# Kernel optimization log

Hardware: AMD Instinct MI355X
Metric: run time of the kernel (lower is better)

Reference implementation:

```python
import jax, jax.numpy as jnp
import numpy as np
from jax import lax

B, T = 64, 512
NUM_C = 2000
SK, AN, H, ATT = 256, 96, 256, 80
D = SK + AN  # LSTM input size


def setup_inputs() -> dict:
    key = jax.random.key(0)
    ks = jax.random.split(key, 10)
    s = 0.05
    skill = jax.random.randint(ks[0], (B, T), 0, NUM_C)
    answer = jax.random.randint(ks[1], (B, T), 0, 2)
    skill_emb = jax.random.normal(ks[2], (NUM_C + 1, SK), jnp.float32) * s
    skill_emb = skill_emb.at[-1].set(0.0)  # padding row zeroed as in __init__
    answer_emb = jax.random.normal(ks[3], (3, AN), jnp.float32) * s
    answer_emb = answer_emb.at[-1].set(0.0)
    Wih = jax.random.normal(ks[4], (4 * H, D), jnp.float32) * s
    Whh = jax.random.normal(ks[5], (4 * H, H), jnp.float32) * s
    bih = jnp.zeros((4 * H,), jnp.float32)
    bhh = jnp.zeros((4 * H,), jnp.float32)
    mlp_w = jax.random.normal(ks[6], (ATT, H), jnp.float32) * s
    mlp_b = jnp.zeros((ATT,), jnp.float32)
    sim_w = jax.random.normal(ks[7], (1, ATT), jnp.float32) * s
    fc_w = jax.random.normal(ks[8], (NUM_C, 2 * H), jnp.float32) * s
    fc_b = jnp.zeros((NUM_C,), jnp.float32)
    return dict(skill=skill, answer=answer, skill_emb=skill_emb, answer_emb=answer_emb,
                Wih=Wih, Whh=Whh, bih=bih, bhh=bhh,
                mlp_w=mlp_w, mlp_b=mlp_b, sim_w=sim_w, fc_w=fc_w, fc_b=fc_b)


def _lstm(x, Wih, Whh, bih, bhh):
    # x: [B,T,D] -> h: [B,T,H], PyTorch gate order (i,f,g,o)
    xg = jnp.einsum('btd,gd->btg', x, Wih) + bih + bhh  # precompute input part
    h0 = jnp.zeros((x.shape[0], H), x.dtype)
    c0 = jnp.zeros((x.shape[0], H), x.dtype)

    def step(carry, xt):
        h, c = carry
        g = xt + h @ Whh.T
        i, f, gg, o = jnp.split(g, 4, axis=-1)
        c = jax.nn.sigmoid(f) * c + jax.nn.sigmoid(i) * jnp.tanh(gg)
        h = jax.nn.sigmoid(o) * jnp.tanh(c)
        return (h, c), h

    _, hs = lax.scan(step, (h0, c0), xg.transpose(1, 0, 2))
    return hs.transpose(1, 0, 2)


def reference(skill, answer, skill_emb, answer_emb, Wih, Whh, bih, bhh,
              mlp_w, mlp_b, sim_w, fc_w, fc_b):
    se = skill_emb[skill]    # [B,T,SK]
    ae = answer_emb[answer]  # [B,T,AN]
    sa = jnp.concatenate([se, ae], axis=-1)
    a_s = jnp.concatenate([ae, se], axis=-1)
    sae = jnp.where((answer == 1)[..., None], sa, a_s)  # [B,T,D]

    h = _lstm(sae, Wih, Whh, bih, bhh)  # [B,T,H]

    # rank-1 causal attention: score per timestep, causal softmax == cumulative ratio
    scores = (jnp.tanh(h @ mlp_w.T + mlp_b) @ sim_w.T)[..., 0]  # [B,T]
    m = jnp.max(scores, axis=1, keepdims=True)
    e = jnp.exp(scores - m)                          # [B,T]
    num = jnp.cumsum(e[..., None] * h, axis=1)       # [B,T,H]
    den = jnp.cumsum(e, axis=1)[..., None]           # [B,T,1]
    attn = num / den                                  # == bmm(softmax(masked scores), h)

    cum1 = jnp.cumsum(attn, axis=1) - attn            # exclusive cumsum
    final = jnp.concatenate([cum1, h], axis=-1)       # [B,T,2H]
    res = jax.nn.sigmoid(final @ fc_w.T + fc_b)       # [B,T,num_c]
    return res, sae
```

## Files before the change

### kernel.cpp

```cpp
#include <hip/hip_runtime.h>
#include <hip/hip_fp16.h>

typedef unsigned int  u32;
typedef unsigned short u16;
typedef _Float16 half_t;
typedef _Float16 f16x8 __attribute__((ext_vector_type(8)));
typedef _Float16 h2    __attribute__((ext_vector_type(2)));
typedef float    f32x4 __attribute__((ext_vector_type(4)));

#define B_   64
#define T_   512
#define NUMC 2000
#define H_   256
#define ATT  80
#define D_   352
#define BT_  32768
#define G4   1024

__device__ __forceinline__ float fdot2f(u32 a, u32 b, float c) {
#if __has_builtin(__builtin_amdgcn_fdot2)
  return __builtin_amdgcn_fdot2(__builtin_bit_cast(h2, a), __builtin_bit_cast(h2, b), c, false);
#else
  h2 ha = __builtin_bit_cast(h2, a), hb = __builtin_bit_cast(h2, b);
  return c + (float)ha.x * (float)hb.x + (float)ha.y * (float)hb.y;
#endif
}

__device__ __forceinline__ void load_lds16(const void* g, void* l) {
  __builtin_amdgcn_global_load_lds((const __attribute__((address_space(1))) void*)g,
                                   (__attribute__((address_space(3))) void*)l, 16, 0, 0);
}

__device__ __forceinline__ u32 pack2f(float x, float y) {
  h2 h; h.x = (_Float16)x; h.y = (_Float16)y;
  return __builtin_bit_cast(u32, h);
}

__device__ __forceinline__ float sigmoidf_(float x) { return 1.f / (1.f + __expf(-x)); }

__device__ __forceinline__ float fast_tanhf(float x) {
  float e = __expf(2.f * x);
  return 1.f - 2.f / (e + 1.f);
}

__device__ __forceinline__ int  sel4i(int4 v, int q) { return q==0?v.x:q==1?v.y:q==2?v.z:v.w; }
__device__ __forceinline__ u32  sel4u(uint4 v, int q){ return q==0?v.x:q==1?v.y:q==2?v.z:v.w; }

__global__ void prep_weights(const float* __restrict__ Wih, const float* __restrict__ mlp_w,
                             const float* __restrict__ fc_w,
                             half_t* __restrict__ wih_h, half_t* __restrict__ mlp_p,
                             half_t* __restrict__ fc_p)
{
  int i = blockIdx.x * 256 + threadIdx.x;
  if (i < 360448) { wih_h[i] = (half_t)Wih[i]; return; }
  i -= 360448;
  if (i < 32768) {
    int row = i >> 8;
    mlp_p[i] = (row < ATT) ? (half_t)mlp_w[i] : (half_t)0.f;
    return;
  }
  i -= 32768;
  if (i < 1048576) {
    int row = i >> 9;
    fc_p[i] = (row < NUMC) ? (half_t)fc_w[i] : (half_t)0.f;
  }
}

__global__ __launch_bounds__(128)
void gather_sae(const int* __restrict__ skill, const int* __restrict__ answer,
                const float* __restrict__ semb, const float* __restrict__ aemb,
                float* __restrict__ sae, half_t* __restrict__ sae_h)
{
  const int tok = blockIdx.x;
  const int tid = threadIdx.x;
  const int s = skill[tok], a = answer[tok];
  float* so = sae + (size_t)tok * D_;
  half_t* ho = sae_h + (size_t)tok * D_;
#pragma unroll
  for (int k = 0; k < 3; ++k) {
    int d = tid + k * 128;
    if (d >= D_) break;
    float v;
    if (a == 1) v = (d < 256) ? semb[s * 256 + d]  : aemb[96 + (d - 256)];
    else        v = (d < 96)  ? aemb[a * 96 + d]   : semb[s * 256 + (d - 96)];
    so[d] = v;
    ho[d] = (half_t)v;
  }
}

template<int EPI>
__global__ __launch_bounds__(256)
void gemm_bt(const half_t* __restrict__ A, const half_t* __restrict__ Bm,
             float* __restrict__ Cf, half_t* __restrict__ Ch,
             const float* __restrict__ b0, const float* __restrict__ b1,
             int K, int N, int Nout)
{
  __shared__ half_t At [128 * 32];
  __shared__ half_t Bt2[128 * 32];
  const int tid  = threadIdx.x;
  const int lane = tid & 63;
  const int wv   = tid >> 6;
  const int m0   = blockIdx.x * 128;
  const int n0   = blockIdx.y * 128;
  const int wm   = (wv & 1) * 64, wn = (wv >> 1) * 64;
  const int lrow = wv * 16 + (lane >> 2);
  const int lk   = (lane & 3) * 8;

  f32x4 acc[4][4];
#pragma unroll
  for (int mi = 0; mi < 4; ++mi)
#pragma unroll
    for (int ni = 0; ni < 4; ++ni) acc[mi][ni] = (f32x4){0.f, 0.f, 0.f, 0.f};

  for (int k0 = 0; k0 < K; k0 += 32) {
    load_lds16(A  + (size_t)(m0 + lrow)      * K + k0 + lk, &At [wv * 512]);
    load_lds16(A  + (size_t)(m0 + 64 + lrow) * K + k0 + lk, &At [2048 + wv * 512]);
    load_lds16(Bm + (size_t)(n0 + lrow)      * K + k0 + lk, &Bt2[wv * 512]);
    load_lds16(Bm + (size_t)(n0 + 64 + lrow) * K + k0 + lk, &Bt2[2048 + wv * 512]);
    __syncthreads();
    f16x8 af[4], bf[4];
#pragma unroll
    for (int mi = 0; mi < 4; ++mi)
      af[mi] = *(const f16x8*)&At [(wm + mi * 16 + (lane & 15)) * 32 + (lane >> 4) * 8];
#pragma unroll
    for (int ni = 0; ni < 4; ++ni)
      bf[ni] = *(const f16x8*)&Bt2[(wn + ni * 16 + (lane & 15)) * 32 + (lane >> 4) * 8];
    __syncthreads();
#pragma unroll
    for (int mi = 0; mi < 4; ++mi)
#pragma unroll
      for (int ni = 0; ni < 4; ++ni)
        acc[mi][ni] = __builtin_amdgcn_mfma_f32_16x16x32_f16(af[mi], bf[ni], acc[mi][ni], 0, 0, 0);
  }

  const int rbase = (lane >> 4) * 4;
  const int cidx  = lane & 15;
#pragma unroll
  for (int mi = 0; mi < 4; ++mi) {
#pragma unroll
    for (int ni = 0; ni < 4; ++ni) {
      int gc = n0 + wn + ni * 16 + cidx;
#pragma unroll
      for (int r = 0; r < 4; ++r) {
        int gr = m0 + wm + mi * 16 + rbase + r;
        float v = acc[mi][ni][r];
        if (EPI == 0) {
          Ch[(size_t)gr * N + gc] = (half_t)(v + b0[gc] + b1[gc]);
        } else if (EPI == 1) {
          Cf[(size_t)gr * N + gc] = v;
        } else {
          if (gc < Nout) Cf[(size_t)gr * Nout + gc] = sigmoidf_(v + b0[gc]);
        }
      }
    }
  }
}

#define RPV 96
__global__ __launch_bounds__(512, 2)
void lstm_kernel(const half_t* __restrict__ xg, const float* __restrict__ Whh,
                 u32* __restrict__ hout )
{
  __shared__ uint4 wlds[8 * 1024];
  __shared__ float gbuf[1024];
  __shared__ __align__(16) u16 hq[256];
  const int tid  = threadIdx.x;
  const int lane = tid & 63;
  const int b    = blockIdx.x;
  const int j0   = tid, j1 = tid + 512;

  u32 wA[RPV], wB[RPV];
#pragma unroll
  for (int p = 0; p < RPV; ++p) {
    float2 a = *(const float2*)&Whh[j0 * 256 + 2 * p];
    float2 c = *(const float2*)&Whh[j1 * 256 + 2 * p];
    wA[p] = pack2f(a.x, a.y);
    wB[p] = pack2f(c.x, c.y);
  }
#pragma unroll
  for (int g = 0; g < 8; ++g) {
    const float* pa = &Whh[j0 * 256 + 2 * (RPV + 4 * g)];
    const float* pb = &Whh[j1 * 256 + 2 * (RPV + 4 * g)];
    uint4 wa, wb;
    wa.x = pack2f(pa[0], pa[1]); wa.y = pack2f(pa[2], pa[3]);
    wa.z = pack2f(pa[4], pa[5]); wa.w = pack2f(pa[6], pa[7]);
    wb.x = pack2f(pb[0], pb[1]); wb.y = pack2f(pb[2], pb[3]);
    wb.z = pack2f(pb[4], pb[5]); wb.w = pack2f(pb[6], pb[7]);
    wlds[g * 1024 + j0] = wa;
    wlds[g * 1024 + j1] = wb;
  }
  if (tid < 128) ((u32*)hq)[tid] = 0u;
  float cst = 0.f;
  const half_t* xrow = xg + (size_t)b * T_ * G4;
  float x0 = (float)xrow[j0], x1 = (float)xrow[j1];
  __syncthreads();

  for (int t = 0; t < T_; ++t) {
    int4 hv = ((const int4*)hq)[lane & 31];
    float acc0 = x0, acc1 = x1;
    if (t < T_ - 1) {
      x0 = (float)xrow[(size_t)(t + 1) * G4 + j0];
      x1 = (float)xrow[(size_t)(t + 1) * G4 + j1];
    }
#pragma unroll
    for (int p = 0; p < RPV; ++p) {
      u32 hp = (u32)__builtin_amdgcn_readlane(sel4i(hv, p & 3), p >> 2);
      acc0 = fdot2f(hp, wA[p], acc0);
      acc1 = fdot2f(hp, wB[p], acc1);
    }
#pragma unroll
    for (int g = 0; g < 8; ++g) {
      uint4 wa = wlds[g * 1024 + j0];
      uint4 wb = wlds[g * 1024 + j1];
#pragma unroll
      for (int q = 0; q < 4; ++q) {
        int p = RPV + 4 * g + q;
        u32 hp = (u32)__builtin_amdgcn_readlane(sel4i(hv, p & 3), p >> 2);
        acc0 = fdot2f(hp, sel4u(wa, q), acc0);
        acc1 = fdot2f(hp, sel4u(wb, q), acc1);
      }
    }
    gbuf[j0] = acc0;
    gbuf[j1] = acc1;
    __syncthreads();
    if (tid < 256) {
      float gi = gbuf[tid], gf = gbuf[tid + 256], gg = gbuf[tid + 512], go = gbuf[tid + 768];
      cst = sigmoidf_(gf) * cst + sigmoidf_(gi) * fast_tanhf(gg);
      float h = sigmoidf_(go) * fast_tanhf(cst);
      hq[tid] = __builtin_bit_cast(u16, (_Float16)h);
    }
    __syncthreads();
    if (tid < 128) hout[(size_t)(b * T_ + t) * 128 + tid] = ((const u32*)hq)[tid];
  }
}

__global__ __launch_bounds__(256)
void attn_kernel(const float* __restrict__ sp , const float* __restrict__ mlp_b,
                 const float* __restrict__ sim_w, const half_t* __restrict__ hh ,
                 half_t* __restrict__ fin )
{
  __shared__ float e[T_];
  __shared__ float red[4];
  const int tid = threadIdx.x;
  const int b   = blockIdx.x;

  float sc0 = 0.f, sc1 = 0.f;
  {
    const float* r0 = sp + (size_t)(b * T_ + tid) * 128;
    const float* r1 = sp + (size_t)(b * T_ + tid + 256) * 128;
    for (int a = 0; a < ATT; ++a) {
      float w = sim_w[a], bb = mlp_b[a];
      sc0 += fast_tanhf(r0[a] + bb) * w;
      sc1 += fast_tanhf(r1[a] + bb) * w;
    }
  }
  float smax = fmaxf(sc0, sc1);
#pragma unroll
  for (int off = 1; off < 64; off <<= 1) smax = fmaxf(smax, __shfl_xor(smax, off, 64));
  if ((tid & 63) == 0) red[tid >> 6] = smax;
  __syncthreads();
  float m = fmaxf(fmaxf(red[0], red[1]), fmaxf(red[2], red[3]));
  e[tid]       = __expf(sc0 - m);
  e[tid + 256] = __expf(sc1 - m);
  __syncthreads();

  float num = 0.f, den = 0.f, c1 = 0.f;
  const half_t* hbase = hh + (size_t)b * T_ * H_ + tid;
  half_t* fbase = fin + (size_t)b * T_ * 512;
  float pre[4];
#pragma unroll
  for (int d = 0; d < 4; ++d) pre[d] = (float)hbase[(size_t)d * H_];
  for (int t = 0; t < T_; ++t) {
    float hv = pre[t & 3];
    if (t + 4 < T_) pre[t & 3] = (float)hbase[(size_t)(t + 4) * H_];
    float et = e[t];
    den += et;
    num += et * hv;
    float attn = num / den;
    half_t* fr = fbase + (size_t)t * 512;
    fr[tid]       = (half_t)c1;
    fr[256 + tid] = (half_t)hv;
    c1 += attn;
  }
}

extern "C" void kernel_launch(void* const* d_in, const int* in_sizes, int n_in,
                              void* d_out, int out_size, void* d_ws, size_t ws_size,
                              hipStream_t stream)
{
  (void)in_sizes; (void)n_in; (void)out_size; (void)ws_size;
  const int*   skill  = (const int*)d_in[0];
  const int*   answer = (const int*)d_in[1];
  const float* semb   = (const float*)d_in[2];
  const float* aemb   = (const float*)d_in[3];
  const float* Wih    = (const float*)d_in[4];
  const float* Whh    = (const float*)d_in[5];
  const float* bih    = (const float*)d_in[6];
  const float* bhh    = (const float*)d_in[7];
  const float* mlp_w  = (const float*)d_in[8];
  const float* mlp_b  = (const float*)d_in[9];
  const float* sim_w  = (const float*)d_in[10];
  const float* fc_w   = (const float*)d_in[11];
  const float* fc_b   = (const float*)d_in[12];

  float* res = (float*)d_out;
  float* sae = (float*)d_out + (size_t)BT_ * NUMC;

  char* ws = (char*)d_ws;
  half_t* sae_h = (half_t*)(ws + 0);
  half_t* wih_h = (half_t*)(ws + 23068672);
  half_t* mlp_p = (half_t*)(ws + 23789568);
  half_t* fc_p  = (half_t*)(ws + 23855104);
  half_t* xg_h  = (half_t*)(ws + 25952256);
  half_t* fin   = (half_t*)(ws + 25952256);
  u32*    h2u   = (u32*)   (ws + 93061120);
  float*  sp    = (float*) (ws + 109838336);

  prep_weights<<<5632, 256, 0, stream>>>(Wih, mlp_w, fc_w, wih_h, mlp_p, fc_p);
  gather_sae<<<BT_, 128, 0, stream>>>(skill, answer, semb, aemb, sae, sae_h);
  gemm_bt<0><<<dim3(256, 8), 256, 0, stream>>>(sae_h, wih_h, nullptr, xg_h, bih, bhh, 352, 1024, 0);
  lstm_kernel<<<64, 512, 0, stream>>>(xg_h, Whh, h2u);
  gemm_bt<1><<<dim3(256, 1), 256, 0, stream>>>((const half_t*)h2u, mlp_p, sp, nullptr, nullptr, nullptr, 256, 128, 0);
  attn_kernel<<<64, 256, 0, stream>>>(sp, mlp_b, sim_w, (const half_t*)h2u, fin);
  gemm_bt<2><<<dim3(256, 16), 256, 0, stream>>>(fin, fc_p, res, nullptr, fc_b, nullptr, 512, 2048, NUMC);
}
```

Measured before the change: 1.995 ms.

## Use one LSTM gate row per thread with 1024-thread blocks

The recurrent LSTM kernel now launches 1024 threads per batch block, so each thread owns one gate row instead of two. It keeps 92 packed half2 weights in registers and the remaining 36 pairs in LDS (9 uint4 groups). Each thread uses two interleaved accumulators to shorten the dependent fdot2 chain. This halves the serial per-thread work per timestep and adds waves to hide latency, at the cost of higher register pressure per wave under the 4-waves-per-EU cap and more threads joining each barrier.

Result: slower. 2.093 ms (+4.9%).

```diff
diff --git a/kernel.cpp b/kernel.cpp
--- a/kernel.cpp
+++ b/kernel.cpp
@@ -156,72 +156,68 @@
   }
 }
 
-#define RPV 96
-__global__ __launch_bounds__(512, 2)
+#define RPV 92
+#define LG  9
+__global__ __launch_bounds__(1024)
+__attribute__((amdgpu_waves_per_eu(4, 4)))
 void lstm_kernel(const half_t* __restrict__ xg, const float* __restrict__ Whh,
                  u32* __restrict__ hout )
 {
-  __shared__ uint4 wlds[8 * 1024];
+  __shared__ uint4 wlds[LG * 1024];
   __shared__ float gbuf[1024];
   __shared__ __align__(16) u16 hq[256];
   const int tid  = threadIdx.x;
   const int lane = tid & 63;
   const int b    = blockIdx.x;
-  const int j0   = tid, j1 = tid + 512;
-
-  u32 wA[RPV], wB[RPV];
-#pragma unroll
-  for (int p = 0; p < RPV; ++p) {
-    float2 a = *(const float2*)&Whh[j0 * 256 + 2 * p];
-    float2 c = *(const float2*)&Whh[j1 * 256 + 2 * p];
-    wA[p] = pack2f(a.x, a.y);
-    wB[p] = pack2f(c.x, c.y);
-  }
-#pragma unroll
-  for (int g = 0; g < 8; ++g) {
-    const float* pa = &Whh[j0 * 256 + 2 * (RPV + 4 * g)];
-    const float* pb = &Whh[j1 * 256 + 2 * (RPV + 4 * g)];
-    uint4 wa, wb;
+
+  u32 wR[RPV];
+  const float* wrow = &Whh[tid * 256];
+#pragma unroll
+  for (int c = 0; c < RPV / 4; ++c) {
+#pragma unroll
+    for (int q = 0; q < 4; ++q) {
+      float2 a = *(const float2*)&wrow[2 * (4 * c + q)];
+      wR[4 * c + q] = pack2f(a.x, a.y);
+    }
+    asm volatile("" ::: "memory");
+  }
+#pragma unroll
+  for (int g = 0; g < LG; ++g) {
+    const float* pa = &wrow[2 * (RPV + 4 * g)];
+    uint4 wa;
     wa.x = pack2f(pa[0], pa[1]); wa.y = pack2f(pa[2], pa[3]);
     wa.z = pack2f(pa[4], pa[5]); wa.w = pack2f(pa[6], pa[7]);
-    wb.x = pack2f(pb[0], pb[1]); wb.y = pack2f(pb[2], pb[3]);
-    wb.z = pack2f(pb[4], pb[5]); wb.w = pack2f(pb[6], pb[7]);
-    wlds[g * 1024 + j0] = wa;
-    wlds[g * 1024 + j1] = wb;
+    wlds[g * 1024 + tid] = wa;
+    asm volatile("" ::: "memory");
   }
   if (tid < 128) ((u32*)hq)[tid] = 0u;
   float cst = 0.f;
   const half_t* xrow = xg + (size_t)b * T_ * G4;
-  float x0 = (float)xrow[j0], x1 = (float)xrow[j1];
+  float x = (float)xrow[tid];
   __syncthreads();
 
   for (int t = 0; t < T_; ++t) {
     int4 hv = ((const int4*)hq)[lane & 31];
-    float acc0 = x0, acc1 = x1;
-    if (t < T_ - 1) {
-      x0 = (float)xrow[(size_t)(t + 1) * G4 + j0];
-      x1 = (float)xrow[(size_t)(t + 1) * G4 + j1];
-    }
+    float acc0 = x, acc1 = 0.f;
+    if (t < T_ - 1) x = (float)xrow[(size_t)(t + 1) * G4 + tid];
 #pragma unroll
     for (int p = 0; p < RPV; ++p) {
       u32 hp = (u32)__builtin_amdgcn_readlane(sel4i(hv, p & 3), p >> 2);
-      acc0 = fdot2f(hp, wA[p], acc0);
-      acc1 = fdot2f(hp, wB[p], acc1);
-    }
-#pragma unroll
-    for (int g = 0; g < 8; ++g) {
-      uint4 wa = wlds[g * 1024 + j0];
-      uint4 wb = wlds[g * 1024 + j1];
+      if (p & 1) acc1 = fdot2f(hp, wR[p], acc1);
+      else       acc0 = fdot2f(hp, wR[p], acc0);
+    }
+#pragma unroll
+    for (int g = 0; g < LG; ++g) {
+      uint4 wa = wlds[g * 1024 + tid];
 #pragma unroll
       for (int q = 0; q < 4; ++q) {
         int p = RPV + 4 * g + q;
         u32 hp = (u32)__builtin_amdgcn_readlane(sel4i(hv, p & 3), p >> 2);
-        acc0 = fdot2f(hp, sel4u(wa, q), acc0);
-        acc1 = fdot2f(hp, sel4u(wb, q), acc1);
+        if (q & 1) acc1 = fdot2f(hp, sel4u(wa, q), acc1);
+        else       acc0 = fdot2f(hp, sel4u(wa, q), acc0);
       }
     }
-    gbuf[j0] = acc0;
-    gbuf[j1] = acc1;
+    gbuf[tid] = acc0 + acc1;
     __syncthreads();
     if (tid < 256) {
       float gi = gbuf[tid], gf = gbuf[tid + 256], gg = gbuf[tid + 512], go = gbuf[tid + 768];
@@ -319,7 +315,7 @@
   prep_weights<<<5632, 256, 0, stream>>>(Wih, mlp_w, fc_w, wih_h, mlp_p, fc_p);
   gather_sae<<<BT_, 128, 0, stream>>>(skill, answer, semb, aemb, sae, sae_h);
   gemm_bt<0><<<dim3(256, 8), 256, 0, stream>>>(sae_h, wih_h, nullptr, xg_h, bih, bhh, 352, 1024, 0);
-  lstm_kernel<<<64, 512, 0, stream>>>(xg_h, Whh, h2u);
+  lstm_kernel<<<64, 1024, 0, stream>>>(xg_h, Whh, h2u);
   gemm_bt<1><<<dim3(256, 1), 256, 0, stream>>>((const half_t*)h2u, mlp_p, sp, nullptr, nullptr, nullptr, 256, 128, 0);
   attn_kernel<<<64, 256, 0, stream>>>(sp, mlp_b, sim_w, (const half_t*)h2u, fin);
   gemm_bt<2><<<dim3(256, 16), 256, 0, stream>>>(fin, fc_p, res, nullptr, fc_b, nullptr, 512, 2048, NUMC);
```
